# Performance work log

Measured on AMD Instinct MI355X. Metric: run time of the kernel, lower is better.

## Reference

```python
import jax, jax.numpy as jnp
import numpy as np

N_NODES = 10000
N_EDGES = 160000
FEAT = 32
EMB = 32
VOCAB = 32000
EDGE_DIM = 9
HID = 32  # edge MLP hidden


def setup_inputs() -> dict:
    key = jax.random.key(0)
    ks = jax.random.split(key, 16)
    s = lambda *sh: 1.0 / np.sqrt(sh[0])
    inp = {
        "signal": jax.random.randint(ks[0], (1,), 0, VOCAB, dtype=jnp.int64) if jax.config.jax_enable_x64 else jax.random.randint(ks[0], (1,), 0, VOCAB).astype(jnp.int32),
        "x": jax.random.normal(ks[1], (N_NODES, FEAT), dtype=jnp.float32),
        "edge_index": jax.random.randint(ks[2], (2, N_EDGES), 0, N_NODES).astype(jnp.int32),
        "edge_attr": jax.random.normal(ks[3], (N_EDGES, EDGE_DIM), dtype=jnp.float32),
        # edge MLP 1: 9 -> 32 -> FEAT*EMB
        "w1a": jax.random.normal(ks[4], (EDGE_DIM, HID), dtype=jnp.float32) * s(EDGE_DIM),
        "b1a": jnp.zeros((HID,), jnp.float32),
        "w1b": jax.random.normal(ks[5], (HID, FEAT * EMB), dtype=jnp.float32) * s(HID),
        "b1b": jnp.zeros((FEAT * EMB,), jnp.float32),
        "root1": jax.random.normal(ks[6], (FEAT, EMB), dtype=jnp.float32) * s(FEAT),
        "bias1": jnp.zeros((EMB,), jnp.float32),
        # edge MLP 2: 9 -> 32 -> EMB*EMB
        "w2a": jax.random.normal(ks[7], (EDGE_DIM, HID), dtype=jnp.float32) * s(EDGE_DIM),
        "b2a": jnp.zeros((HID,), jnp.float32),
        "w2b": jax.random.normal(ks[8], (HID, EMB * EMB), dtype=jnp.float32) * s(HID),
        "b2b": jnp.zeros((EMB * EMB,), jnp.float32),
        "root2": jax.random.normal(ks[9], (EMB, EMB), dtype=jnp.float32) * s(EMB),
        "bias2": jnp.zeros((EMB,), jnp.float32),
        "emb_table": jax.random.normal(ks[10], (VOCAB, EMB), dtype=jnp.float32),
    }
    return inp


def nnconv(x, edge_index, edge_attr, wa, ba, wb, bb, root, bias, in_ch, out_ch):
    # edge MLP -> per-edge weight matrices [E, in_ch, out_ch]
    h = jax.nn.relu(edge_attr @ wa + ba)
    W_e = (h @ wb + bb).reshape(-1, in_ch, out_ch)
    src, dst = edge_index[0], edge_index[1]
    # gather source node features, per-edge matmul
    msg = jnp.einsum("ei,eio->eo", x[src], W_e)  # [E, out_ch]
    summed = jax.ops.segment_sum(msg, dst, num_segments=N_NODES)
    cnt = jax.ops.segment_sum(jnp.ones((msg.shape[0],), msg.dtype), dst, num_segments=N_NODES)
    aggr = summed / jnp.maximum(cnt, 1.0)[:, None]  # scatter-mean (0 for isolated nodes)
    return aggr + x @ root + bias


def reference(signal, x, edge_index, edge_attr,
              w1a, b1a, w1b, b1b, root1, bias1,
              w2a, b2a, w2b, b2b, root2, bias2, emb_table):
    h = jax.nn.relu(nnconv(x, edge_index, edge_attr, w1a, b1a, w1b, b1b, root1, bias1, FEAT, EMB))
    h = jax.nn.relu(nnconv(h, edge_index, edge_attr, w2a, b2a, w2b, b2b, root2, bias2, EMB, EMB))
    sig = emb_table[signal]          # [1, EMB]
    sig = sig[0]                      # squeeze leading 1 (matches torch branch)
    scores = h @ sig                  # [N]
    return jax.nn.log_softmax(scores, axis=0)
```

## Files before the change

### kernel.cpp

```cpp
#include <hip/hip_runtime.h>
#include <math.h>

#define NN 10000
#define NE 160000
#define C  32
#define ED 9
#define EAP 12

typedef __attribute__((ext_vector_type(8))) short short8v;
typedef __attribute__((ext_vector_type(4))) float float4v;

__device__ inline unsigned short f2bf(float f) {
    unsigned int u = __float_as_uint(f);
    return (unsigned short)((u + 0x7fffu + ((u >> 16) & 1u)) >> 16);
}

#define ZB 655
__global__ __launch_bounds__(256) void prep_kernel(uint4* __restrict__ zreg, int n16,
                                                   const float* __restrict__ w1b,
                                                   const float* __restrict__ w2b,
                                                   float* __restrict__ wbT1,
                                                   float* __restrict__ wbT2) {
    const int b = blockIdx.x, tid = threadIdx.x;
    if (b < ZB) {
        const int i = b * 256 + tid;
        if (i < n16) zreg[i] = uint4{0u, 0u, 0u, 0u};
    } else if (b < ZB + 128) {
        const int idx = (b - ZB) * 256 + tid;
        const int i = idx & 31, k = (idx >> 5) & 31, o = idx >> 10;
        wbT1[idx] = w1b[k * (C * C) + i * C + o];
    } else {
        const int idx = (b - ZB - 128) * 256 + tid;
        const int i = idx & 31, k = (idx >> 5) & 31, o = idx >> 10;
        wbT2[idx] = w2b[k * (C * C) + i * C + o];
    }
}

__global__ __launch_bounds__(256) void hist_kernel(const int* __restrict__ ei,
                                                   int* __restrict__ cnt_src,
                                                   int* __restrict__ cnt_dst) {
    const int e = blockIdx.x * 256 + threadIdx.x;
    if (e < NE) {
        atomicAdd(&cnt_src[ei[e]], 1);
        atomicAdd(&cnt_dst[ei[NE + e]], 1);
    }
}

__global__ __launch_bounds__(1024) void scan_kernel(const int* __restrict__ cnt,
                                                    int* __restrict__ offs) {
    __shared__ int wtot[16];
    const int t = threadIdx.x;
    const int lane = t & 63, wid = t >> 6;
    const int base = t * 10;
    int loc[10];
    int s = 0;
#pragma unroll
    for (int j = 0; j < 10; ++j) {
        int v = (base + j < NN) ? cnt[base + j] : 0;
        loc[j] = s;
        s += v;
    }
    int inc = s;
    for (int d = 1; d < 64; d <<= 1) {
        int v = __shfl_up(inc, d, 64);
        if (lane >= d) inc += v;
    }
    if (lane == 63) wtot[wid] = inc;
    __syncthreads();
    if (t < 16) {
        int w = wtot[t];
        for (int d = 1; d < 16; d <<= 1) {
            int v = __shfl_up(w, d, 64);
            if (t >= d) w += v;
        }
        wtot[t] = w;
    }
    __syncthreads();
    const int excl = inc - s + (wid ? wtot[wid - 1] : 0);
#pragma unroll
    for (int j = 0; j < 10; ++j)
        if (base + j < NN) offs[base + j] = excl + loc[j];
    if (t == 1023) offs[NN] = wtot[15];
}

__global__ __launch_bounds__(256) void scatter_kernel(const int* __restrict__ ei,
                                                      const float* __restrict__ ea,
                                                      const int* __restrict__ offs,
                                                      int* __restrict__ cursor,
                                                      int* __restrict__ dst_s,
                                                      float* __restrict__ ea_s) {
    const int e = blockIdx.x * 256 + threadIdx.x;
    if (e < NE) {
        const int b   = ei[e];
        const int pos = offs[b] + atomicAdd(&cursor[b], 1);
        dst_s[pos] = ei[NE + e];
#pragma unroll
        for (int j = 0; j < ED; ++j)
            ea_s[(size_t)pos * EAP + j] = ea[(size_t)e * ED + j];
    }
}

__global__ __launch_bounds__(256) void u_gemm2(const float* __restrict__ xin,
                                               const float* __restrict__ wbT,
                                               const float* __restrict__ bb,
                                               unsigned short* __restrict__ UT,
                                               float* __restrict__ xb) {
    __shared__ float xs[16 * C];
    const int b   = blockIdx.x;
    const int nb  = (b >> 2) * 16;
    const int o0  = (b & 3) * 8;
    const int tid = threadIdx.x;
    for (int t = tid; t < 16 * C; t += 256) xs[t] = xin[nb * C + t];
    __syncthreads();

    const int op = tid >> 5, k = tid & 31, o = o0 + op;
    float4v wv[8];
    const float* wp = wbT + ((size_t)o * C + k) * C;
#pragma unroll
    for (int i4 = 0; i4 < 8; ++i4)
        wv[i4] = *reinterpret_cast<const float4v*>(wp + i4 * 4);

#pragma unroll
    for (int n = 0; n < 16; ++n) {
        float acc = 0.f;
#pragma unroll
        for (int i4 = 0; i4 < 8; ++i4) {
            const float4v xv = *reinterpret_cast<const float4v*>(&xs[n * C + i4 * 4]);
            acc += xv.x * wv[i4].x + xv.y * wv[i4].y + xv.z * wv[i4].z + xv.w * wv[i4].w;
        }
        UT[(size_t)(nb + n) * (C * C) + o * C + k] = f2bf(acc);
    }
    if (o0 == 0) {
#pragma unroll
        for (int t = 0; t < 2; ++t) {
            const int idx = t * 256 + tid;
            const int n = idx >> 5, oo = idx & 31;
            float acc = 0.f;
#pragma unroll
            for (int i = 0; i < C; ++i) acc += xs[n * C + i] * bb[i * C + oo];
            xb[(nb + n) * C + oo] = acc;
        }
    }
}

__global__ __launch_bounds__(256) void u_gemm2_fused(const float* __restrict__ xin,
                                                     const float* __restrict__ sumbuf1,
                                                     const int* __restrict__ cnt,
                                                     const float* __restrict__ root1,
                                                     const float* __restrict__ bias1,
                                                     const float* __restrict__ wbT,
                                                     const float* __restrict__ bb,
                                                     unsigned short* __restrict__ UT,
                                                     float* __restrict__ xb,
                                                     float* __restrict__ h1out) {
    __shared__ float xs[16 * C];
    __shared__ float hs[16 * C];
    const int b   = blockIdx.x;
    const int nb  = (b >> 2) * 16;
    const int o0  = (b & 3) * 8;
    const int tid = threadIdx.x;
    for (int t = tid; t < 16 * C; t += 256) xs[t] = xin[nb * C + t];
    __syncthreads();

#pragma unroll
    for (int t = 0; t < 2; ++t) {
        const int idx = t * 256 + tid;
        const int n = idx >> 5, oo = idx & 31;
        float acc = bias1[oo];
#pragma unroll
        for (int i = 0; i < C; ++i) acc += xs[n * C + i] * root1[i * C + oo];
        const float cn = fmaxf((float)cnt[nb + n], 1.f);
        acc += sumbuf1[(size_t)(nb + n) * C + oo] / cn;
        const float h = fmaxf(acc, 0.f);
        hs[n * C + oo] = h;
        if (o0 == 0) h1out[(size_t)(nb + n) * C + oo] = h;
    }
    __syncthreads();

    const int op = tid >> 5, k = tid & 31, o = o0 + op;
    float4v wv[8];
    const float* wp = wbT + ((size_t)o * C + k) * C;
#pragma unroll
    for (int i4 = 0; i4 < 8; ++i4)
        wv[i4] = *reinterpret_cast<const float4v*>(wp + i4 * 4);

#pragma unroll
    for (int n = 0; n < 16; ++n) {
        float acc = 0.f;
#pragma unroll
        for (int i4 = 0; i4 < 8; ++i4) {
            const float4v xv = *reinterpret_cast<const float4v*>(&hs[n * C + i4 * 4]);
            acc += xv.x * wv[i4].x + xv.y * wv[i4].y + xv.z * wv[i4].z + xv.w * wv[i4].w;
        }
        UT[(size_t)(nb + n) * (C * C) + o * C + k] = f2bf(acc);
    }
    if (o0 == 0) {
#pragma unroll
        for (int t = 0; t < 2; ++t) {
            const int idx = t * 256 + tid;
            const int n = idx >> 5, oo = idx & 31;
            float acc = 0.f;
#pragma unroll
            for (int i = 0; i < C; ++i) acc += hs[n * C + i] * bb[i * C + oo];
            xb[(size_t)(nb + n) * C + oo] = acc;
        }
    }
}

__global__ __launch_bounds__(256) void edge4_kernel(const int* __restrict__ offs,
                                                    const int* __restrict__ dst_s,
                                                    const float* __restrict__ ea_s,
                                                    const float* __restrict__ wa,
                                                    const float* __restrict__ ba,
                                                    const unsigned short* __restrict__ UT,
                                                    const float* __restrict__ xb,
                                                    float* __restrict__ sumbuf) {
    __shared__ float was[ED * C];
    __shared__ float bas[C];
    const int tid = threadIdx.x;
    for (int t = tid; t < ED * C; t += 256) was[t] = wa[t];
    if (tid < C) bas[tid] = ba[tid];
    __syncthreads();

    const int w  = tid >> 6;
    const int l  = tid & 63;
    const int s  = blockIdx.x * 4 + w;
    const int q  = l >> 4;
    const int el = l & 15;

    const int e0 = offs[s], e1 = offs[s + 1];
    if (e0 == e1) return;

    const unsigned short* up = UT + (size_t)s * (C * C);
    const short8v B1 = *reinterpret_cast<const short8v*>(up + el * C + q * 8);
    const short8v B2 = *reinterpret_cast<const short8v*>(up + (el + 16) * C + q * 8);
    const float c1 = xb[s * C + el];
    const float c2 = xb[s * C + el + 16];
    const float4v C1 = {c1, c1, c1, c1};
    const float4v C2 = {c2, c2, c2, c2};
    float hb[8];
#pragma unroll
    for (int i = 0; i < 8; ++i) hb[i] = bas[q * 8 + i];

    for (int pb = e0; pb < e1; pb += 16) {
        const int p  = pb + el;
        const int pc = (p < e1) ? p : e0;
        const float* eap = ea_s + (size_t)pc * EAP;
        const float4v ea0 = *reinterpret_cast<const float4v*>(eap);
        const float4v ea1 = *reinterpret_cast<const float4v*>(eap + 4);
        const float   ea8 = eap[8];

        float h[8];
#pragma unroll
        for (int i = 0; i < 8; ++i) h[i] = hb[i];
#pragma unroll
        for (int j = 0; j < ED; ++j) {
            const float ev = (j == 0) ? ea0.x : (j == 1) ? ea0.y : (j == 2) ? ea0.z
                           : (j == 3) ? ea0.w : (j == 4) ? ea1.x : (j == 5) ? ea1.y
                           : (j == 6) ? ea1.z : (j == 7) ? ea1.w : ea8;
            const float4v w0 = *reinterpret_cast<const float4v*>(&was[j * C + q * 8]);
            const float4v w1 = *reinterpret_cast<const float4v*>(&was[j * C + q * 8 + 4]);
            h[0] += ev * w0.x; h[1] += ev * w0.y; h[2] += ev * w0.z; h[3] += ev * w0.w;
            h[4] += ev * w1.x; h[5] += ev * w1.y; h[6] += ev * w1.z; h[7] += ev * w1.w;
        }
        union { int u[4]; short8v v; } A;
#pragma unroll
        for (int v = 0; v < 4; ++v) {
            const unsigned lo = f2bf(fmaxf(h[2 * v], 0.f));
            const unsigned hi = f2bf(fmaxf(h[2 * v + 1], 0.f));
            A.u[v] = (int)(lo | (hi << 16));
        }
        const float4v d1 = __builtin_amdgcn_mfma_f32_16x16x32_bf16(A.v, B1, C1, 0, 0, 0);
        const float4v d2 = __builtin_amdgcn_mfma_f32_16x16x32_bf16(A.v, B2, C2, 0, 0, 0);
#pragma unroll
        for (int r = 0; r < 4; ++r) {
            const int pe = pb + q * 4 + r;
            if (pe < e1) {
                const int dst = dst_s[pe];
                atomicAdd(&sumbuf[(size_t)dst * C + el],      d1[r]);
                atomicAdd(&sumbuf[(size_t)dst * C + el + 16], d2[r]);
            }
        }
    }
}

__global__ __launch_bounds__(256) void node2_score(const float* __restrict__ h1,
                                                   const float* __restrict__ sumbuf,
                                                   const int* __restrict__ cnt,
                                                   const float* __restrict__ root,
                                                   const float* __restrict__ bias,
                                                   const float* __restrict__ emb,
                                                   const int* __restrict__ signal,
                                                   float* __restrict__ scores) {
    __shared__ float rs[C * C];
    __shared__ float bs[C];
    __shared__ float sig[C];
    __shared__ float xs[8][C];
    const int tid = threadIdx.x;
    for (int t = tid; t < C * C; t += 256) rs[t] = root[t];
    if (tid < C) {
        bs[tid]  = bias[tid];
        sig[tid] = emb[(size_t)signal[0] * C + tid];
    }
    const int nl = tid >> 5, o = tid & 31;
    const int n  = blockIdx.x * 8 + nl;
    xs[nl][o] = h1[(size_t)n * C + o];
    __syncthreads();
    float acc = bs[o];
#pragma unroll
    for (int i = 0; i < C; ++i) acc += xs[nl][i] * rs[i * C + o];
    const float cn = fmaxf((float)cnt[n], 1.f);
    acc += sumbuf[(size_t)n * C + o] / cn;
    float val = fmaxf(acc, 0.f) * sig[o];
#pragma unroll
    for (int off = 16; off; off >>= 1) val += __shfl_xor(val, off, 32);
    if (o == 0) scores[n] = val;
}

__global__ __launch_bounds__(1024) void reduce_out_kernel(const float* __restrict__ scores,
                                                          float* __restrict__ out) {
    __shared__ float sm[16];
    __shared__ float ss[16];
    const int tid = threadIdx.x;
    float m = -INFINITY;
    for (int n = tid; n < NN; n += 1024) m = fmaxf(m, scores[n]);
    for (int off = 32; off; off >>= 1) m = fmaxf(m, __shfl_down(m, off, 64));
    if ((tid & 63) == 0) sm[tid >> 6] = m;
    __syncthreads();
    if (tid == 0) {
        float mm = sm[0];
        for (int w = 1; w < 16; ++w) mm = fmaxf(mm, sm[w]);
        sm[0] = mm;
    }
    __syncthreads();
    const float gmax = sm[0];
    float s = 0.f;
    for (int n = tid; n < NN; n += 1024) s += expf(scores[n] - gmax);
    for (int off = 32; off; off >>= 1) s += __shfl_down(s, off, 64);
    if ((tid & 63) == 0) ss[tid >> 6] = s;
    __syncthreads();
    if (tid == 0) {
        float t = 0.f;
        for (int w = 0; w < 16; ++w) t += ss[w];
        ss[0] = logf(t);
    }
    __syncthreads();
    const float sub = gmax + ss[0];
    for (int n = tid; n < NN; n += 1024) out[n] = scores[n] - sub;
}

extern "C" void kernel_launch(void* const* d_in, const int* in_sizes, int n_in,
                              void* d_out, int out_size, void* d_ws, size_t ws_size,
                              hipStream_t stream) {
    const int*   signal = (const int*)d_in[0];
    const float* x      = (const float*)d_in[1];
    const int*   ei     = (const int*)d_in[2];
    const float* ea     = (const float*)d_in[3];
    const float* w1a    = (const float*)d_in[4];
    const float* b1a    = (const float*)d_in[5];
    const float* w1b    = (const float*)d_in[6];
    const float* b1b    = (const float*)d_in[7];
    const float* root1  = (const float*)d_in[8];
    const float* bias1  = (const float*)d_in[9];
    const float* w2a    = (const float*)d_in[10];
    const float* b2a    = (const float*)d_in[11];
    const float* w2b    = (const float*)d_in[12];
    const float* b2b    = (const float*)d_in[13];
    const float* root2  = (const float*)d_in[14];
    const float* bias2  = (const float*)d_in[15];
    const float* emb    = (const float*)d_in[16];

    float* ws = (float*)d_ws;
    unsigned short* UT = (unsigned short*)ws;
    float* xb      = ws + 5120000;
    float* h1      = xb + NN * C;
    float* ea_s    = h1 + NN * C;
    float* wbT1    = ea_s + (size_t)NE * EAP;
    float* wbT2    = wbT1 + 32768;
    float* scores  = wbT2 + 32768;
    float* sumbuf1 = scores + NN;
    float* sumbuf2 = sumbuf1 + NN * C;
    int*   cnt_src = (int*)(sumbuf2 + NN * C);
    int*   cnt_dst = cnt_src + NN;
    int*   cursor  = cnt_dst + NN;
    int*   offs    = cursor + NN;
    int*   dst_s   = offs + NN + 16;

    const int n16 = 167500;

    prep_kernel<<<ZB + 256, 256, 0, stream>>>((uint4*)sumbuf1, n16, w1b, w2b, wbT1, wbT2);
    hist_kernel<<<(NE + 255) / 256, 256, 0, stream>>>(ei, cnt_src, cnt_dst);
    scan_kernel<<<1, 1024, 0, stream>>>(cnt_src, offs);
    scatter_kernel<<<(NE + 255) / 256, 256, 0, stream>>>(ei, ea, offs, cursor, dst_s, ea_s);
    u_gemm2<<<2500, 256, 0, stream>>>(x, wbT1, b1b, UT, xb);
    edge4_kernel<<<2500, 256, 0, stream>>>(offs, dst_s, ea_s, w1a, b1a, UT, xb, sumbuf1);
    u_gemm2_fused<<<2500, 256, 0, stream>>>(x, sumbuf1, cnt_dst, root1, bias1,
                                            wbT2, b2b, UT, xb, h1);
    edge4_kernel<<<2500, 256, 0, stream>>>(offs, dst_s, ea_s, w2a, b2a, UT, xb, sumbuf2);
    node2_score<<<1250, 256, 0, stream>>>(h1, sumbuf2, cnt_dst, root2, bias2,
                                          emb, signal, scores);
    reduce_out_kernel<<<1, 1024, 0, stream>>>(scores, (float*)d_out);
}
```

Baseline: 161.1 us.

## Replace atomic scatter-add with dst-sorted message buffer and segmented node reduction

Edges are sorted by destination as well as source. The edge kernels now write each message to its dst-sorted slot, with no float atomics into a sum buffer. New node-aggregation kernels then reduce contiguous message segments and apply the root/bias/relu. The scatter pass is fused with the first U-GEMM, the two scans run in one launch, and the softmax is folded into the last node kernel through a last-block counter. This removes atomic contention and some launches, at the cost of an extra 20MB message buffer written and read per layer.

New measurement: 340.7 us. +111.5%, slower.

```diff
diff --git a/kernel.cpp b/kernel.cpp
--- a/kernel.cpp
+++ b/kernel.cpp
@@ -15,22 +15,22 @@
     return (unsigned short)((u + 0x7fffu + ((u >> 16) & 1u)) >> 16);
 }
 
-#define ZB 655
-__global__ __launch_bounds__(256) void prep_kernel(uint4* __restrict__ zreg, int n16,
+#define ZQ 10016
+__global__ __launch_bounds__(256) void prep_kernel(uint4* __restrict__ zreg,
                                                    const float* __restrict__ w1b,
                                                    const float* __restrict__ w2b,
                                                    float* __restrict__ wbT1,
                                                    float* __restrict__ wbT2) {
     const int b = blockIdx.x, tid = threadIdx.x;
-    if (b < ZB) {
+    if (b < 40) {
         const int i = b * 256 + tid;
-        if (i < n16) zreg[i] = uint4{0u, 0u, 0u, 0u};
-    } else if (b < ZB + 128) {
-        const int idx = (b - ZB) * 256 + tid;
+        if (i < ZQ) zreg[i] = uint4{0u, 0u, 0u, 0u};
+    } else if (b < 168) {
+        const int idx = (b - 40) * 256 + tid;
         const int i = idx & 31, k = (idx >> 5) & 31, o = idx >> 10;
         wbT1[idx] = w1b[k * (C * C) + i * C + o];
     } else {
-        const int idx = (b - ZB - 128) * 256 + tid;
+        const int idx = (b - 168) * 256 + tid;
         const int i = idx & 31, k = (idx >> 5) & 31, o = idx >> 10;
         wbT2[idx] = w2b[k * (C * C) + i * C + o];
     }
@@ -46,8 +46,12 @@
     }
 }
 
-__global__ __launch_bounds__(1024) void scan_kernel(const int* __restrict__ cnt,
-                                                    int* __restrict__ offs) {
+__global__ __launch_bounds__(1024) void scan2_kernel(const int* __restrict__ cnt_src,
+                                                     const int* __restrict__ cnt_dst,
+                                                     int* __restrict__ offs,
+                                                     int* __restrict__ doffs) {
+    const int* cnt = blockIdx.x ? cnt_dst : cnt_src;
+    int* out       = blockIdx.x ? doffs   : offs;
     __shared__ int wtot[16];
     const int t = threadIdx.x;
     const int lane = t & 63, wid = t >> 6;
@@ -79,24 +83,80 @@
     const int excl = inc - s + (wid ? wtot[wid - 1] : 0);
 #pragma unroll
     for (int j = 0; j < 10; ++j)
-        if (base + j < NN) offs[base + j] = excl + loc[j];
-    if (t == 1023) offs[NN] = wtot[15];
-}
-
-__global__ __launch_bounds__(256) void scatter_kernel(const int* __restrict__ ei,
-                                                      const float* __restrict__ ea,
-                                                      const int* __restrict__ offs,
-                                                      int* __restrict__ cursor,
-                                                      int* __restrict__ dst_s,
-                                                      float* __restrict__ ea_s) {
-    const int e = blockIdx.x * 256 + threadIdx.x;
-    if (e < NE) {
-        const int b   = ei[e];
-        const int pos = offs[b] + atomicAdd(&cursor[b], 1);
-        dst_s[pos] = ei[NE + e];
-#pragma unroll
-        for (int j = 0; j < ED; ++j)
-            ea_s[(size_t)pos * EAP + j] = ea[(size_t)e * ED + j];
+        if (base + j < NN) out[base + j] = excl + loc[j];
+    if (t == 1023) out[NN] = wtot[15];
+}
+
+__device__ __forceinline__ void u_body(int vb, int tid, float* __restrict__ xs,
+                                       const float* __restrict__ xin,
+                                       const float* __restrict__ wbT,
+                                       const float* __restrict__ bb,
+                                       unsigned short* __restrict__ UT,
+                                       float* __restrict__ xb) {
+    const int nb = (vb >> 2) * 16;
+    const int o0 = (vb & 3) * 8;
+    for (int t = tid; t < 16 * C; t += 256) xs[t] = xin[nb * C + t];
+    __syncthreads();
+
+    const int op = tid >> 5, k = tid & 31, o = o0 + op;
+    float4v wv[8];
+    const float* wp = wbT + ((size_t)o * C + k) * C;
+#pragma unroll
+    for (int i4 = 0; i4 < 8; ++i4)
+        wv[i4] = *reinterpret_cast<const float4v*>(wp + i4 * 4);
+
+#pragma unroll
+    for (int n = 0; n < 16; ++n) {
+        float acc = 0.f;
+#pragma unroll
+        for (int i4 = 0; i4 < 8; ++i4) {
+            const float4v xv = *reinterpret_cast<const float4v*>(&xs[n * C + i4 * 4]);
+            acc += xv.x * wv[i4].x + xv.y * wv[i4].y + xv.z * wv[i4].z + xv.w * wv[i4].w;
+        }
+        UT[(size_t)(nb + n) * (C * C) + o * C + k] = f2bf(acc);
+    }
+    if (o0 == 0) {
+#pragma unroll
+        for (int t = 0; t < 2; ++t) {
+            const int idx = t * 256 + tid;
+            const int n = idx >> 5, oo = idx & 31;
+            float acc = 0.f;
+#pragma unroll
+            for (int i = 0; i < C; ++i) acc += xs[n * C + i] * bb[i * C + oo];
+            xb[(size_t)(nb + n) * C + oo] = acc;
+        }
+    }
+}
+
+__global__ __launch_bounds__(256) void mid_kernel(const int* __restrict__ ei,
+                                                  const float* __restrict__ ea,
+                                                  const int* __restrict__ offs,
+                                                  const int* __restrict__ doffs,
+                                                  int* __restrict__ cur_src,
+                                                  int* __restrict__ cur_dst,
+                                                  int* __restrict__ pd,
+                                                  float* __restrict__ ea_s,
+                                                  const float* __restrict__ xin,
+                                                  const float* __restrict__ wbT,
+                                                  const float* __restrict__ bb,
+                                                  unsigned short* __restrict__ UT,
+                                                  float* __restrict__ xb) {
+    __shared__ float xs[16 * C];
+    const int b = blockIdx.x, tid = threadIdx.x;
+    if (b < 625) {
+        const int e = b * 256 + tid;
+        if (e < NE) {
+            const int sn  = ei[e];
+            const int dn  = ei[NE + e];
+            const int pos = offs[sn]  + atomicAdd(&cur_src[sn], 1);
+            const int dpo = doffs[dn] + atomicAdd(&cur_dst[dn], 1);
+            pd[pos] = dpo;
+#pragma unroll
+            for (int j = 0; j < ED; ++j)
+                ea_s[(size_t)pos * EAP + j] = ea[(size_t)e * ED + j];
+        }
+    } else {
+        u_body(b - 625, tid, xs, xin, wbT, bb, UT, xb);
     }
 }
 
@@ -106,115 +166,17 @@
                                                unsigned short* __restrict__ UT,
                                                float* __restrict__ xb) {
     __shared__ float xs[16 * C];
-    const int b   = blockIdx.x;
-    const int nb  = (b >> 2) * 16;
-    const int o0  = (b & 3) * 8;
-    const int tid = threadIdx.x;
-    for (int t = tid; t < 16 * C; t += 256) xs[t] = xin[nb * C + t];
-    __syncthreads();
-
-    const int op = tid >> 5, k = tid & 31, o = o0 + op;
-    float4v wv[8];
-    const float* wp = wbT + ((size_t)o * C + k) * C;
-#pragma unroll
-    for (int i4 = 0; i4 < 8; ++i4)
-        wv[i4] = *reinterpret_cast<const float4v*>(wp + i4 * 4);
-
-#pragma unroll
-    for (int n = 0; n < 16; ++n) {
-        float acc = 0.f;
-#pragma unroll
-        for (int i4 = 0; i4 < 8; ++i4) {
-            const float4v xv = *reinterpret_cast<const float4v*>(&xs[n * C + i4 * 4]);
-            acc += xv.x * wv[i4].x + xv.y * wv[i4].y + xv.z * wv[i4].z + xv.w * wv[i4].w;
-        }
-        UT[(size_t)(nb + n) * (C * C) + o * C + k] = f2bf(acc);
-    }
-    if (o0 == 0) {
-#pragma unroll
-        for (int t = 0; t < 2; ++t) {
-            const int idx = t * 256 + tid;
-            const int n = idx >> 5, oo = idx & 31;
-            float acc = 0.f;
-#pragma unroll
-            for (int i = 0; i < C; ++i) acc += xs[n * C + i] * bb[i * C + oo];
-            xb[(nb + n) * C + oo] = acc;
-        }
-    }
-}
-
-__global__ __launch_bounds__(256) void u_gemm2_fused(const float* __restrict__ xin,
-                                                     const float* __restrict__ sumbuf1,
-                                                     const int* __restrict__ cnt,
-                                                     const float* __restrict__ root1,
-                                                     const float* __restrict__ bias1,
-                                                     const float* __restrict__ wbT,
-                                                     const float* __restrict__ bb,
-                                                     unsigned short* __restrict__ UT,
-                                                     float* __restrict__ xb,
-                                                     float* __restrict__ h1out) {
-    __shared__ float xs[16 * C];
-    __shared__ float hs[16 * C];
-    const int b   = blockIdx.x;
-    const int nb  = (b >> 2) * 16;
-    const int o0  = (b & 3) * 8;
-    const int tid = threadIdx.x;
-    for (int t = tid; t < 16 * C; t += 256) xs[t] = xin[nb * C + t];
-    __syncthreads();
-
-#pragma unroll
-    for (int t = 0; t < 2; ++t) {
-        const int idx = t * 256 + tid;
-        const int n = idx >> 5, oo = idx & 31;
-        float acc = bias1[oo];
-#pragma unroll
-        for (int i = 0; i < C; ++i) acc += xs[n * C + i] * root1[i * C + oo];
-        const float cn = fmaxf((float)cnt[nb + n], 1.f);
-        acc += sumbuf1[(size_t)(nb + n) * C + oo] / cn;
-        const float h = fmaxf(acc, 0.f);
-        hs[n * C + oo] = h;
-        if (o0 == 0) h1out[(size_t)(nb + n) * C + oo] = h;
-    }
-    __syncthreads();
-
-    const int op = tid >> 5, k = tid & 31, o = o0 + op;
-    float4v wv[8];
-    const float* wp = wbT + ((size_t)o * C + k) * C;
-#pragma unroll
-    for (int i4 = 0; i4 < 8; ++i4)
-        wv[i4] = *reinterpret_cast<const float4v*>(wp + i4 * 4);
-
-#pragma unroll
-    for (int n = 0; n < 16; ++n) {
-        float acc = 0.f;
-#pragma unroll
-        for (int i4 = 0; i4 < 8; ++i4) {
-            const float4v xv = *reinterpret_cast<const float4v*>(&hs[n * C + i4 * 4]);
-            acc += xv.x * wv[i4].x + xv.y * wv[i4].y + xv.z * wv[i4].z + xv.w * wv[i4].w;
-        }
-        UT[(size_t)(nb + n) * (C * C) + o * C + k] = f2bf(acc);
-    }
-    if (o0 == 0) {
-#pragma unroll
-        for (int t = 0; t < 2; ++t) {
-            const int idx = t * 256 + tid;
-            const int n = idx >> 5, oo = idx & 31;
-            float acc = 0.f;
-#pragma unroll
-            for (int i = 0; i < C; ++i) acc += hs[n * C + i] * bb[i * C + oo];
-            xb[(size_t)(nb + n) * C + oo] = acc;
-        }
-    }
-}
-
-__global__ __launch_bounds__(256) void edge4_kernel(const int* __restrict__ offs,
-                                                    const int* __restrict__ dst_s,
+    u_body(blockIdx.x, threadIdx.x, xs, xin, wbT, bb, UT, xb);
+}
+
+__global__ __launch_bounds__(256) void edge5_kernel(const int* __restrict__ offs,
+                                                    const int* __restrict__ pd,
                                                     const float* __restrict__ ea_s,
                                                     const float* __restrict__ wa,
                                                     const float* __restrict__ ba,
                                                     const unsigned short* __restrict__ UT,
                                                     const float* __restrict__ xb,
-                                                    float* __restrict__ sumbuf) {
+                                                    float* __restrict__ msg) {
     __shared__ float was[ED * C];
     __shared__ float bas[C];
     const int tid = threadIdx.x;
@@ -276,77 +238,111 @@
         for (int r = 0; r < 4; ++r) {
             const int pe = pb + q * 4 + r;
             if (pe < e1) {
-                const int dst = dst_s[pe];
-                atomicAdd(&sumbuf[(size_t)dst * C + el],      d1[r]);
-                atomicAdd(&sumbuf[(size_t)dst * C + el + 16], d2[r]);
+                const int mr = pd[pe];
+                msg[(size_t)mr * C + el]      = d1[r];
+                msg[(size_t)mr * C + el + 16] = d2[r];
             }
         }
     }
 }
 
-__global__ __launch_bounds__(256) void node2_score(const float* __restrict__ h1,
-                                                   const float* __restrict__ sumbuf,
-                                                   const int* __restrict__ cnt,
-                                                   const float* __restrict__ root,
-                                                   const float* __restrict__ bias,
-                                                   const float* __restrict__ emb,
-                                                   const int* __restrict__ signal,
-                                                   float* __restrict__ scores) {
+__global__ __launch_bounds__(256) void nodeagg1_kernel(const int* __restrict__ doffs,
+                                                       const float* __restrict__ msg,
+                                                       const float* __restrict__ xin,
+                                                       const float* __restrict__ root,
+                                                       const float* __restrict__ bias,
+                                                       float* __restrict__ h1out) {
+    __shared__ float rs[C * C];
+    __shared__ float bs[C];
+    __shared__ float xls[4][C];
+    const int tid = threadIdx.x;
+    for (int t = tid; t < C * C; t += 256) rs[t] = root[t];
+    if (tid < C) bs[tid] = bias[tid];
+    __syncthreads();
+
+    const int w = tid >> 6, lane = tid & 63;
+    const int half = lane >> 5, o = lane & 31;
+    const int d = blockIdx.x * 4 + w;
+    const int e0 = doffs[d], e1 = doffs[d + 1];
+
+    float acc = 0.f;
+    for (int p = e0 + half; p < e1; p += 2) acc += msg[(size_t)p * C + o];
+    acc += __shfl_down(acc, 32, 64);
+    if (lane < 32) xls[w][o] = xin[(size_t)d * C + o];
+    if (lane < 32) {
+        const float cn = fmaxf((float)(e1 - e0), 1.f);
+        float a = bs[o] + acc / cn;
+#pragma unroll
+        for (int i = 0; i < C; ++i) a += xls[w][i] * rs[i * C + o];
+        h1out[(size_t)d * C + o] = fmaxf(a, 0.f);
+    }
+}
+
+__global__ __launch_bounds__(256) void nodeagg2_out(const int* __restrict__ doffs,
+                                                    const float* __restrict__ msg,
+                                                    const float* __restrict__ h1,
+                                                    const float* __restrict__ root,
+                                                    const float* __restrict__ bias,
+                                                    const float* __restrict__ emb,
+                                                    const int* __restrict__ signal,
+                                                    float* __restrict__ scores,
+                                                    int* __restrict__ counter,
+                                                    float* __restrict__ out) {
     __shared__ float rs[C * C];
     __shared__ float bs[C];
     __shared__ float sig[C];
-    __shared__ float xs[8][C];
+    __shared__ float xls[4][C];
+    __shared__ int   is_last;
+    __shared__ float sm[4];
     const int tid = threadIdx.x;
     for (int t = tid; t < C * C; t += 256) rs[t] = root[t];
     if (tid < C) {
         bs[tid]  = bias[tid];
         sig[tid] = emb[(size_t)signal[0] * C + tid];
     }
-    const int nl = tid >> 5, o = tid & 31;
-    const int n  = blockIdx.x * 8 + nl;
-    xs[nl][o] = h1[(size_t)n * C + o];
-    __syncthreads();
-    float acc = bs[o];
-#pragma unroll
-    for (int i = 0; i < C; ++i) acc += xs[nl][i] * rs[i * C + o];
-    const float cn = fmaxf((float)cnt[n], 1.f);
-    acc += sumbuf[(size_t)n * C + o] / cn;
-    float val = fmaxf(acc, 0.f) * sig[o];
-#pragma unroll
-    for (int off = 16; off; off >>= 1) val += __shfl_xor(val, off, 32);
-    if (o == 0) scores[n] = val;
-}
-
-__global__ __launch_bounds__(1024) void reduce_out_kernel(const float* __restrict__ scores,
-                                                          float* __restrict__ out) {
-    __shared__ float sm[16];
-    __shared__ float ss[16];
-    const int tid = threadIdx.x;
+    __syncthreads();
+
+    const int w = tid >> 6, lane = tid & 63;
+    const int half = lane >> 5, o = lane & 31;
+    const int d = blockIdx.x * 4 + w;
+    const int e0 = doffs[d], e1 = doffs[d + 1];
+
+    float acc = 0.f;
+    for (int p = e0 + half; p < e1; p += 2) acc += msg[(size_t)p * C + o];
+    acc += __shfl_down(acc, 32, 64);
+    if (lane < 32) xls[w][o] = h1[(size_t)d * C + o];
+    if (lane < 32) {
+        const float cn = fmaxf((float)(e1 - e0), 1.f);
+        float a = bs[o] + acc / cn;
+#pragma unroll
+        for (int i = 0; i < C; ++i) a += xls[w][i] * rs[i * C + o];
+        float val = fmaxf(a, 0.f) * sig[o];
+#pragma unroll
+        for (int off = 16; off; off >>= 1) val += __shfl_xor(val, off, 32);
+        if (o == 0) scores[d] = val;
+    }
+
+    __threadfence();
+    if (tid == 0) is_last = (atomicAdd(counter, 1) == gridDim.x - 1);
+    __syncthreads();
+    if (!is_last) return;
+    __threadfence();
+
     float m = -INFINITY;
-    for (int n = tid; n < NN; n += 1024) m = fmaxf(m, scores[n]);
+    for (int n = tid; n < NN; n += 256) m = fmaxf(m, scores[n]);
+#pragma unroll
     for (int off = 32; off; off >>= 1) m = fmaxf(m, __shfl_down(m, off, 64));
-    if ((tid & 63) == 0) sm[tid >> 6] = m;
-    __syncthreads();
-    if (tid == 0) {
-        float mm = sm[0];
-        for (int w = 1; w < 16; ++w) mm = fmaxf(mm, sm[w]);
-        sm[0] = mm;
-    }
-    __syncthreads();
-    const float gmax = sm[0];
+    if (lane == 0) sm[w] = m;
+    __syncthreads();
+    const float gmax = fmaxf(fmaxf(sm[0], sm[1]), fmaxf(sm[2], sm[3]));
     float s = 0.f;
-    for (int n = tid; n < NN; n += 1024) s += expf(scores[n] - gmax);
+    for (int n = tid; n < NN; n += 256) s += expf(scores[n] - gmax);
+#pragma unroll
     for (int off = 32; off; off >>= 1) s += __shfl_down(s, off, 64);
-    if ((tid & 63) == 0) ss[tid >> 6] = s;
-    __syncthreads();
-    if (tid == 0) {
-        float t = 0.f;
-        for (int w = 0; w < 16; ++w) t += ss[w];
-        ss[0] = logf(t);
-    }
-    __syncthreads();
-    const float sub = gmax + ss[0];
-    for (int n = tid; n < NN; n += 1024) out[n] = scores[n] - sub;
+    if (lane == 0) sm[w] = s;
+    __syncthreads();
+    const float sub = gmax + logf(sm[0] + sm[1] + sm[2] + sm[3]);
+    for (int n = tid; n < NN; n += 256) out[n] = scores[n] - sub;
 }
 
 extern "C" void kernel_launch(void* const* d_in, const int* in_sizes, int n_in,
@@ -372,32 +368,31 @@
 
     float* ws = (float*)d_ws;
     unsigned short* UT = (unsigned short*)ws;
-    float* xb      = ws + 5120000;
-    float* h1      = xb + NN * C;
-    float* ea_s    = h1 + NN * C;
-    float* wbT1    = ea_s + (size_t)NE * EAP;
+    float* msg     = ws + 5120000;
+    float* xb      = msg + 5120000;
+    float* h1      = xb + 320000;
+    float* ea_s    = h1 + 320000;
+    float* wbT1    = ea_s + 1920000;
     float* wbT2    = wbT1 + 32768;
     float* scores  = wbT2 + 32768;
-    float* sumbuf1 = scores + NN;
-    float* sumbuf2 = sumbuf1 + NN * C;
-    int*   cnt_src = (int*)(sumbuf2 + NN * C);
+    int*   offs    = (int*)(scores + 10000);
+    int*   doffs   = offs + 10016;
+    int*   pd      = doffs + 10016;
+    int*   cnt_src = pd + 160000;
     int*   cnt_dst = cnt_src + NN;
-    int*   cursor  = cnt_dst + NN;
-    int*   offs    = cursor + NN;
-    int*   dst_s   = offs + NN + 16;
-
-    const int n16 = 167500;
-
-    prep_kernel<<<ZB + 256, 256, 0, stream>>>((uint4*)sumbuf1, n16, w1b, w2b, wbT1, wbT2);
+    int*   cur_src = cnt_dst + NN;
+    int*   cur_dst = cur_src + NN;
+    int*   counter = cur_dst + NN;
+
+    prep_kernel<<<296, 256, 0, stream>>>((uint4*)cnt_src, w1b, w2b, wbT1, wbT2);
     hist_kernel<<<(NE + 255) / 256, 256, 0, stream>>>(ei, cnt_src, cnt_dst);
-    scan_kernel<<<1, 1024, 0, stream>>>(cnt_src, offs);
-    scatter_kernel<<<(NE + 255) / 256, 256, 0, stream>>>(ei, ea, offs, cursor, dst_s, ea_s);
-    u_gemm2<<<2500, 256, 0, stream>>>(x, wbT1, b1b, UT, xb);
-    edge4_kernel<<<2500, 256, 0, stream>>>(offs, dst_s, ea_s, w1a, b1a, UT, xb, sumbuf1);
-    u_gemm2_fused<<<2500, 256, 0, stream>>>(x, sumbuf1, cnt_dst, root1, bias1,
-                                            wbT2, b2b, UT, xb, h1);
-    edge4_kernel<<<2500, 256, 0, stream>>>(offs, dst_s, ea_s, w2a, b2a, UT, xb, sumbuf2);
-    node2_score<<<1250, 256, 0, stream>>>(h1, sumbuf2, cnt_dst, root2, bias2,
-                                          emb, signal, scores);
-    reduce_out_kernel<<<1, 1024, 0, stream>>>(scores, (float*)d_out);
-}
+    scan2_kernel<<<2, 1024, 0, stream>>>(cnt_src, cnt_dst, offs, doffs);
+    mid_kernel<<<3125, 256, 0, stream>>>(ei, ea, offs, doffs, cur_src, cur_dst,
+                                         pd, ea_s, x, wbT1, b1b, UT, xb);
+    edge5_kernel<<<2500, 256, 0, stream>>>(offs, pd, ea_s, w1a, b1a, UT, xb, msg);
+    nodeagg1_kernel<<<2500, 256, 0, stream>>>(doffs, msg, x, root1, bias1, h1);
+    u_gemm2<<<2500, 256, 0, stream>>>(h1, wbT2, b2b, UT, xb);
+    edge5_kernel<<<2500, 256, 0, stream>>>(offs, pd, ea_s, w2a, b2a, UT, xb, msg);
+    nodeagg2_out<<<2500, 256, 0, stream>>>(doffs, msg, h1, root2, bias2,
+                                           emb, signal, scores, counter, (float*)d_out);
+}
```
